# Performance work log

Hardware: AMD Instinct MI355X
Metric: run time of the kernel (lower is better)

The kernel has to match this reference:

```python
import jax, jax.numpy as jnp
import numpy as np

B = 2048   # structures
A = 512    # atoms per structure (constant)
N = B * A  # total atoms
O = 48     # symmetry operations


def setup_inputs() -> dict:
    key = jax.random.key(0)
    k1, k2, k3, k4, k5 = jax.random.split(key, 5)
    lattices = jax.random.normal(k1, (B, 3, 3), jnp.float32)
    inv_lattices = jax.random.normal(k2, (B, 3, 3), jnp.float32)
    forces = jax.random.normal(k3, (N, 3), jnp.float32)
    general_ops = jax.random.normal(k4, (O, 4, 4), jnp.float32)
    # scatter targets; in practice these permute atoms within a structure,
    # but any in-range index gives the same math/memory pattern
    symm_map = jax.random.randint(k5, (N, O), 0, N, dtype=jnp.int32)
    num_atoms = jnp.full((B,), A, dtype=jnp.int64)
    num_general_ops = jnp.full((B,), O, dtype=jnp.int64)
    return {
        "lattices": lattices,
        "inv_lattices": inv_lattices,
        "forces": forces,
        "num_atoms": num_atoms,
        "general_ops": general_ops,
        "symm_map": symm_map,
        "num_general_ops": num_general_ops,
    }


def reference(lattices, inv_lattices, forces, num_atoms, general_ops, symm_map, num_general_ops):
    n = forces.shape[0]
    # per-atom lattices via repeat_interleave(num_atoms)
    lat = jnp.repeat(lattices, num_atoms, axis=0, total_repeat_length=n)       # [N,3,3]
    inv_lat = jnp.repeat(inv_lattices, num_atoms, axis=0, total_repeat_length=n)
    # fractional (scaled) forces: einsum('nji,nj->ni')
    scaled = jnp.einsum('nji,nj->ni', inv_lat, forces)                          # [N,3]
    # apply every symmetry rotation at once (vectorized over the op loop)
    rot = general_ops[:, :3, :3]                                                # [O,3,3]
    transformed = jnp.einsum('oij,nj->oni', rot, scaled)                        # [O,N,3]
    # scatter-add each op's transformed forces to symm_map[:, iop] targets
    tgt = symm_map.T.reshape(-1)                                                # [O*N]
    acc = jnp.zeros_like(scaled).at[tgt].add(transformed.reshape(-1, 3))        # [N,3]
    # normalize by number of ops of each atom's structure
    counts = jnp.repeat(num_general_ops, num_atoms, axis=0, total_repeat_length=n)
    sym_scaled = acc / counts.astype(scaled.dtype)[:, None]
    # back to cartesian: einsum('nji,nj->ni') with lattices
    return jnp.einsum('nji,nj->ni', lat, sym_scaled)
```

## Files before the change

kernel.cpp:

```cpp
#include <hip/hip_runtime.h>
#include <math.h>

#define BLOCK 256
#define PBLOCK 1024
#define NB 256
#define TILE 4096
#define GP 512
#define KSLICE 4
#define KS_TOT (KSLICE + 1)
#define GPK (GP / KSLICE)
#define CAPS 27
#define ABLOCK 512
#define AWAVES (ABLOCK / 64)

__global__ void scan_offsets_kernel(const int* __restrict__ num_atoms, int B,
                                    int* __restrict__ offsets) {
    __shared__ long long partial[1024];
    int t = threadIdx.x;
    int per = (B + 1023) / 1024;
    int base_idx = t * per;
    long long local = 0;
    for (int i = 0; i < per; ++i) {
        int idx = base_idx + i;
        if (idx < B) local += num_atoms[idx];
    }
    partial[t] = local;
    __syncthreads();
    for (int d = 1; d < 1024; d <<= 1) {
        long long v = (t >= d) ? partial[t - d] : 0;
        __syncthreads();
        partial[t] += v;
        __syncthreads();
    }
    long long run = (t == 0) ? 0 : partial[t - 1];
    for (int i = 0; i < per; ++i) {
        int idx = base_idx + i;
        if (idx < B) {
            offsets[idx] = (int)run;
            run += num_atoms[idx];
        }
    }
    if (t == 1023) offsets[B] = (int)partial[1023];
}

__device__ __forceinline__ int find_batch(const int* __restrict__ offsets, int B, int n) {
    int lo = 0, hi = B;
    while (hi - lo > 1) {
        int mid = (lo + hi) >> 1;
        if (offsets[mid] <= n) lo = mid; else hi = mid;
    }
    return lo;
}

__global__ void scale_kernel(const float* __restrict__ inv_lat,
                             const float* __restrict__ forces,
                             const int* __restrict__ offsets, int B, int N,
                             float4* __restrict__ scaled, float* __restrict__ partials,
                             int zf, int zt) {
    int n = blockIdx.x * blockDim.x + threadIdx.x;
    if (n >= N) return;
    int b = find_batch(offsets, B, n);
    const float* M = inv_lat + (size_t)b * 9;
    float f0 = forces[n * 3 + 0], f1 = forces[n * 3 + 1], f2 = forces[n * 3 + 2];
    float s0 = M[0] * f0 + M[3] * f1 + M[6] * f2;
    float s1 = M[1] * f0 + M[4] * f1 + M[7] * f2;
    float s2 = M[2] * f0 + M[5] * f1 + M[8] * f2;
    scaled[n] = make_float4(s0, s1, s2, 0.f);
    for (int k = zf; k < zt; ++k) {
        float* a = partials + (size_t)k * N * 3;
        a[n * 3 + 0] = 0.f; a[n * 3 + 1] = 0.f; a[n * 3 + 2] = 0.f;
    }
}

__device__ __forceinline__ int bucket_of(int tgt, int N) {
    return (int)(((unsigned long long)(unsigned)tgt * (unsigned)NB) / (unsigned)N);
}

__global__ __launch_bounds__(PBLOCK, 8) void place_kernel(
                             const int* __restrict__ symm_map,
                             const float4* __restrict__ scaled,
                             const float* __restrict__ general_ops,
                             int atom_base, int atom_cnt, int N, int O, int cap,
                             uint2* __restrict__ records, int* __restrict__ cnts,
                             float* __restrict__ ovf) {
    __shared__ int scnt[NB];
    __shared__ int gcur[NB];
    __shared__ uint2 stage[NB * CAPS];
    int tid = threadIdx.x, g = blockIdx.x;
    int G = PBLOCK / O;
    int active = G * O;
    int grp = tid / O;
    int o = tid - grp * O;
    float r0 = 0, r1 = 0, r2 = 0, r3 = 0, r4 = 0, r5 = 0, r6 = 0, r7 = 0, r8 = 0;
    if (tid < active) {
        const float* Ro = general_ops + (size_t)o * 16;
        r0 = Ro[0]; r1 = Ro[1]; r2 = Ro[2];
        r3 = Ro[4]; r4 = Ro[5]; r5 = Ro[6];
        r6 = Ro[8]; r7 = Ro[9]; r8 = Ro[10];
    }
    for (int i = tid; i < NB; i += PBLOCK) {
        gcur[i] = (int)(((size_t)g * NB + i) * (size_t)cap);
        scnt[i] = 0;
    }
    __syncthreads();
    int apb = (atom_cnt + GP - 1) / GP;
    int a0 = atom_base + g * apb;
    int aend = atom_base + atom_cnt;
    int a1 = a0 + apb; if (a1 > aend) a1 = aend;
    int myAtoms = a1 - a0; if (myAtoms < 0) myAtoms = 0;
    int rstep = G * 4;
    int rounds = (myAtoms + rstep - 1) / rstep;

    for (int r = 0; r < rounds; ++r) {
        if (tid < active) {
            int abase = a0 + r * rstep + grp;
            #pragma unroll
            for (int j = 0; j < 4; ++j) {
                int a = abase + j * G;
                if (a < a1) {
                    int tgt = symm_map[(size_t)a * (size_t)O + (size_t)o];
                    float4 s = scaled[a];
                    float v0 = r0 * s.x + r1 * s.y + r2 * s.z;
                    float v1 = r3 * s.x + r4 * s.y + r5 * s.z;
                    float v2 = r6 * s.x + r7 * s.y + r8 * s.z;
                    float m = fmaxf(fmaxf(fabsf(v0), fabsf(v1)), fabsf(v2));
                    int bb = bucket_of(tgt, N);
                    bool done = false;
                    if (m < 15.9f) {
                        int pos = atomicAdd(&scnt[bb], 1);
                        if (pos < CAPS) {
                            unsigned q0 = (unsigned)(int)rintf(v0 * 32.f + 512.f);
                            unsigned q1 = (unsigned)(int)rintf(v1 * 32.f + 512.f);
                            unsigned q2 = (unsigned)(int)rintf(v2 * 32.f + 512.f);
                            stage[bb * CAPS + pos] =
                                make_uint2(q0 | (q1 << 16),
                                           q2 | (((unsigned)tgt & 0xFFFFu) << 16));
                            done = true;
                        }
                    }
                    if (!done) {
                        atomicAdd(&ovf[(size_t)tgt * 3 + 0], v0);
                        atomicAdd(&ovf[(size_t)tgt * 3 + 1], v1);
                        atomicAdd(&ovf[(size_t)tgt * 3 + 2], v2);
                    }
                }
            }
        }
        __syncthreads();
        int ib = tid >> 4;
        int j = tid & 15;
        for (int pass = 0; pass < NB; pass += PBLOCK / 16) {
            int ii = pass + ib;
            int c = scnt[ii]; if (c > CAPS) c = CAPS;
            int gb = gcur[ii];
            int lim = (int)(((size_t)g * NB + ii + 1) * (size_t)cap);
            int room = lim - gb;
            int w = (c < room) ? c : room; if (w < 0) w = 0;
            for (int k = j; k < w; k += 16)
                records[(size_t)gb + k] = stage[ii * CAPS + k];
            for (int k = w + j; k < c; k += 16) {
                uint2 f = stage[ii * CAPS + k];
                int lo = (int)(((long long)ii * N + NB - 1) / NB);
                int tgt = lo + ((((int)(f.y >> 16)) - (lo & 0xFFFF)) & 0xFFFF);
                float v0 = (float)((int)(f.x & 0xFFFF) - 512) * 0.03125f;
                float v1 = (float)((int)(f.x >> 16) - 512) * 0.03125f;
                float v2 = (float)((int)(f.y & 0xFFFF) - 512) * 0.03125f;
                atomicAdd(&ovf[(size_t)tgt * 3 + 0], v0);
                atomicAdd(&ovf[(size_t)tgt * 3 + 1], v1);
                atomicAdd(&ovf[(size_t)tgt * 3 + 2], v2);
            }
            if (j == 0) { gcur[ii] = gb + w; scnt[ii] = 0; }
        }
        __syncthreads();
    }
    for (int i = tid; i < NB; i += PBLOCK) {
        int base = (int)(((size_t)g * NB + i) * (size_t)cap);
        int c = gcur[i] - base;
        if (c > cap) c = cap;
        if (c < 0) c = 0;
        cnts[(size_t)g * NB + i] = c;
    }
}

__device__ __forceinline__ void accum_rec(unsigned long long* accL,
                                          unsigned x, unsigned y, int lo16) {
    int local = ((int)(y >> 16) - lo16) & 0xFFFF;
    unsigned long long u = (1ULL << 54)
                         | ((unsigned long long)(x & 0xFFFFu) << 36)
                         | ((unsigned long long)(x >> 16) << 18)
                         | (unsigned long long)(y & 0xFFFFu);
    (void)__hip_atomic_fetch_add(&accL[local], u, __ATOMIC_RELAXED, __HIP_MEMORY_SCOPE_WORKGROUP);
}

__global__ __launch_bounds__(ABLOCK) void accum_kernel(const uint2* __restrict__ records,
                             const int* __restrict__ cnts, int N, int cap,
                             float* __restrict__ partials, int store_mode) {
    __shared__ unsigned long long accL[TILE];
    int b = blockIdx.x / KSLICE;
    int k = blockIdx.x - b * KSLICE;
    int tid = threadIdx.x;
    int lo = (int)(((long long)b * N + NB - 1) / NB);
    int hi = (int)(((long long)(b + 1) * N + NB - 1) / NB);
    if (hi > N) hi = N;
    int span = hi - lo;
    for (int i = tid; i < span; i += ABLOCK) accL[i] = 0ULL;
    __syncthreads();
    int lo16 = lo & 0xFFFF;
    int g0 = k * GPK;
    int wave = tid >> 6;
    int lane = tid & 63;
    for (int g = g0 + wave; g < g0 + GPK; g += AWAVES) {
        int c = cnts[(size_t)g * NB + b];
        const uint2* r = records + ((size_t)g * NB + b) * (size_t)cap;
        const uint4* r4 = (const uint4*)r;
        int pairs = c >> 1;
        for (int i = lane; i < pairs; i += 64) {
            uint4 f = r4[i];
            accum_rec(accL, f.x, f.y, lo16);
            accum_rec(accL, f.z, f.w, lo16);
        }
        if (lane == 0 && (c & 1)) {
            uint2 f = r[c - 1];
            accum_rec(accL, f.x, f.y, lo16);
        }
    }
    __syncthreads();
    float* gp = partials + (size_t)k * N * 3 + (size_t)lo * 3;
    for (int t = tid; t < span; t += ABLOCK) {
        unsigned long long u = accL[t];
        int cc = (int)(unsigned)(u >> 54);
        int q0 = (int)((u >> 36) & 0x3FFFF);
        int q1 = (int)((u >> 18) & 0x3FFFF);
        int q2 = (int)(u & 0x3FFFF);
        float f0 = (float)(q0 - 512 * cc) * 0.03125f;
        float f1 = (float)(q1 - 512 * cc) * 0.03125f;
        float f2 = (float)(q2 - 512 * cc) * 0.03125f;
        if (store_mode) {
            gp[t * 3 + 0] = f0; gp[t * 3 + 1] = f1; gp[t * 3 + 2] = f2;
        } else {
            gp[t * 3 + 0] += f0; gp[t * 3 + 1] += f1; gp[t * 3 + 2] += f2;
        }
    }
}

__global__ void scatter_kernel(const float4* __restrict__ scaled,
                               const float* __restrict__ general_ops,
                               const int* __restrict__ symm_map,
                               float* __restrict__ acc,
                               long long total, int O) {
    long long t = (long long)blockIdx.x * blockDim.x + threadIdx.x;
    if (t >= total) return;
    long long n = t / O;
    int o = (int)(t - n * O);
    float4 s = scaled[n];
    const float* R = general_ops + (size_t)o * 16;
    float v0 = R[0] * s.x + R[1] * s.y + R[2] * s.z;
    float v1 = R[4] * s.x + R[5] * s.y + R[6] * s.z;
    float v2 = R[8] * s.x + R[9] * s.y + R[10] * s.z;
    int tgt = symm_map[t];
    atomicAdd(&acc[(size_t)tgt * 3 + 0], v0);
    atomicAdd(&acc[(size_t)tgt * 3 + 1], v1);
    atomicAdd(&acc[(size_t)tgt * 3 + 2], v2);
}

__global__ void output_kernel(const float* __restrict__ lat,
                              const int* __restrict__ num_general_ops,
                              const int* __restrict__ offsets, int B, int N,
                              const float* __restrict__ partials, int K,
                              float* __restrict__ out) {
    int n = blockIdx.x * blockDim.x + threadIdx.x;
    if (n >= N) return;
    int b = find_batch(offsets, B, n);
    float inv_cnt = 1.0f / (float)num_general_ops[b];
    float a0 = 0.f, a1 = 0.f, a2 = 0.f;
    for (int k = 0; k < K; ++k) {
        const float* a = partials + (size_t)k * N * 3;
        a0 += a[n * 3 + 0]; a1 += a[n * 3 + 1]; a2 += a[n * 3 + 2];
    }
    a0 *= inv_cnt; a1 *= inv_cnt; a2 *= inv_cnt;
    const float* M = lat + (size_t)b * 9;
    out[n * 3 + 0] = M[0] * a0 + M[3] * a1 + M[6] * a2;
    out[n * 3 + 1] = M[1] * a0 + M[4] * a1 + M[7] * a2;
    out[n * 3 + 2] = M[2] * a0 + M[5] * a1 + M[8] * a2;
}

static inline size_t align16(size_t x) { return (x + 15) & ~(size_t)15; }

extern "C" void kernel_launch(void* const* d_in, const int* in_sizes, int n_in,
                              void* d_out, int out_size, void* d_ws, size_t ws_size,
                              hipStream_t stream) {
    const float* lattices        = (const float*)d_in[0];
    const float* inv_lattices    = (const float*)d_in[1];
    const float* forces          = (const float*)d_in[2];
    const int*   num_atoms       = (const int*)d_in[3];
    const float* general_ops     = (const float*)d_in[4];
    const int*   symm_map        = (const int*)d_in[5];
    const int*   num_general_ops = (const int*)d_in[6];

    int B = in_sizes[0] / 9;
    int N = in_sizes[2] / 3;
    int O = in_sizes[4] / 16;
    long long total = (long long)N * O;

    char* p = (char*)d_ws;
    size_t used = 0;
    float4* scaled  = (float4*)(p + used); used = align16(used + (size_t)N * sizeof(float4));
    float* partials = (float*)(p + used);  used = align16(used + (size_t)KS_TOT * N * 3 * sizeof(float));
    int* offsets    = (int*)(p + used);    used = align16(used + (size_t)(B + 1) * sizeof(int));
    int* cnts       = (int*)(p + used);    used = align16(used + (size_t)NB * GP * sizeof(int));
    size_t remaining = (ws_size > used) ? ws_size - used : 0;

    int C = -1, cap = 0, chunk_atoms = 0;
    for (int c = 1; c <= 64; ++c) {
        int ca = (N + c - 1) / c;
        int apb = (ca + GP - 1) / GP;
        double m = (double)apb * (double)O / (double)NB;
        long long capc = (long long)(m + 5.0 * sqrt(m > 1.0 ? m : 1.0) + 16.0);
        capc = (capc + 7) & ~7LL;
        if ((size_t)NB * (size_t)GP * (size_t)capc * sizeof(uint2) <= remaining) {
            C = c; cap = (int)capc; chunk_atoms = ca; break;
        }
    }
    bool fast = (C > 0) && (((long long)N + NB - 1) / NB <= TILE) && (O <= 64)
                && (total < (1LL << 31))
                && ((long long)NB * GP * cap < (1LL << 31));

    int gridN = (N + BLOCK - 1) / BLOCK;
    scan_offsets_kernel<<<1, 1024, 0, stream>>>(num_atoms, B, offsets);

    if (fast) {
        uint2* records = (uint2*)(p + used);
        float* ovf = partials + (size_t)KSLICE * N * 3;
        int store_mode = (C == 1) ? 1 : 0;
        int zf = store_mode ? KSLICE : 0;
        scale_kernel<<<gridN, BLOCK, 0, stream>>>(inv_lattices, forces, offsets, B, N,
                                                  scaled, partials, zf, KS_TOT);
        for (int c = 0; c < C; ++c) {
            int abase = c * chunk_atoms;
            if (abase >= N) break;
            int acnt = N - abase;
            if (acnt > chunk_atoms) acnt = chunk_atoms;
            place_kernel<<<GP, PBLOCK, 0, stream>>>(symm_map, scaled, general_ops,
                                                    abase, acnt, N, O, cap,
                                                    records, cnts, ovf);
            accum_kernel<<<NB * KSLICE, ABLOCK, 0, stream>>>(records, cnts, N, cap,
                                                             partials, store_mode);
        }
        output_kernel<<<gridN, BLOCK, 0, stream>>>(lattices, num_general_ops, offsets, B, N,
                                                   partials, KS_TOT, (float*)d_out);
    } else {
        scale_kernel<<<gridN, BLOCK, 0, stream>>>(inv_lattices, forces, offsets, B, N,
                                                  scaled, partials, 0, 1);
        long long gridS = (total + BLOCK - 1) / BLOCK;
        scatter_kernel<<<(int)gridS, BLOCK, 0, stream>>>(scaled, general_ops, symm_map, partials, total, O);
        output_kernel<<<gridN, BLOCK, 0, stream>>>(lattices, num_general_ops, offsets, B, N,
                                                   partials, 1, (float*)d_out);
    }
}
```

Measured before the change: 670.1 us.

## Accumulate each chunk into its own slice and force at least five chunks

```diff
diff --git a/kernel.cpp b/kernel.cpp
--- a/kernel.cpp
+++ b/kernel.cpp
@@ -6,12 +6,9 @@
 #define NB 256
 #define TILE 4096
 #define GP 512
-#define KSLICE 4
-#define KS_TOT (KSLICE + 1)
-#define GPK (GP / KSLICE)
+#define KSMAX 8
 #define CAPS 27
-#define ABLOCK 512
-#define AWAVES (ABLOCK / 64)
+#define ABLOCK 1024
 
 __global__ void scan_offsets_kernel(const int* __restrict__ num_atoms, int B,
                                     int* __restrict__ offsets) {
@@ -194,10 +191,9 @@
 
 __global__ __launch_bounds__(ABLOCK) void accum_kernel(const uint2* __restrict__ records,
                              const int* __restrict__ cnts, int N, int cap,
-                             float* __restrict__ partials, int store_mode) {
+                             float* __restrict__ slice) {
     __shared__ unsigned long long accL[TILE];
-    int b = blockIdx.x / KSLICE;
-    int k = blockIdx.x - b * KSLICE;
+    int b = blockIdx.x;
     int tid = threadIdx.x;
     int lo = (int)(((long long)b * N + NB - 1) / NB);
     int hi = (int)(((long long)(b + 1) * N + NB - 1) / NB);
@@ -206,10 +202,10 @@
     for (int i = tid; i < span; i += ABLOCK) accL[i] = 0ULL;
     __syncthreads();
     int lo16 = lo & 0xFFFF;
-    int g0 = k * GPK;
     int wave = tid >> 6;
     int lane = tid & 63;
-    for (int g = g0 + wave; g < g0 + GPK; g += AWAVES) {
+    const int NW = ABLOCK / 64;
+    for (int g = wave; g < GP; g += NW) {
         int c = cnts[(size_t)g * NB + b];
         const uint2* r = records + ((size_t)g * NB + b) * (size_t)cap;
         const uint4* r4 = (const uint4*)r;
@@ -225,21 +221,16 @@
         }
     }
     __syncthreads();
-    float* gp = partials + (size_t)k * N * 3 + (size_t)lo * 3;
+    float* gp = slice + (size_t)lo * 3;
     for (int t = tid; t < span; t += ABLOCK) {
         unsigned long long u = accL[t];
         int cc = (int)(unsigned)(u >> 54);
         int q0 = (int)((u >> 36) & 0x3FFFF);
         int q1 = (int)((u >> 18) & 0x3FFFF);
         int q2 = (int)(u & 0x3FFFF);
-        float f0 = (float)(q0 - 512 * cc) * 0.03125f;
-        float f1 = (float)(q1 - 512 * cc) * 0.03125f;
-        float f2 = (float)(q2 - 512 * cc) * 0.03125f;
-        if (store_mode) {
-            gp[t * 3 + 0] = f0; gp[t * 3 + 1] = f1; gp[t * 3 + 2] = f2;
-        } else {
-            gp[t * 3 + 0] += f0; gp[t * 3 + 1] += f1; gp[t * 3 + 2] += f2;
-        }
+        gp[t * 3 + 0] = (float)(q0 - 512 * cc) * 0.03125f;
+        gp[t * 3 + 1] = (float)(q1 - 512 * cc) * 0.03125f;
+        gp[t * 3 + 2] = (float)(q2 - 512 * cc) * 0.03125f;
     }
 }
 
@@ -305,13 +296,13 @@
     char* p = (char*)d_ws;
     size_t used = 0;
     float4* scaled  = (float4*)(p + used); used = align16(used + (size_t)N * sizeof(float4));
-    float* partials = (float*)(p + used);  used = align16(used + (size_t)KS_TOT * N * 3 * sizeof(float));
+    float* partials = (float*)(p + used);  used = align16(used + (size_t)(KSMAX + 1) * N * 3 * sizeof(float));
     int* offsets    = (int*)(p + used);    used = align16(used + (size_t)(B + 1) * sizeof(int));
     int* cnts       = (int*)(p + used);    used = align16(used + (size_t)NB * GP * sizeof(int));
     size_t remaining = (ws_size > used) ? ws_size - used : 0;
 
     int C = -1, cap = 0, chunk_atoms = 0;
-    for (int c = 1; c <= 64; ++c) {
+    for (int c = 5; c <= KSMAX; ++c) {
         int ca = (N + c - 1) / c;
         int apb = (ca + GP - 1) / GP;
         double m = (double)apb * (double)O / (double)NB;
@@ -330,11 +321,9 @@
 
     if (fast) {
         uint2* records = (uint2*)(p + used);
-        float* ovf = partials + (size_t)KSLICE * N * 3;
-        int store_mode = (C == 1) ? 1 : 0;
-        int zf = store_mode ? KSLICE : 0;
+        float* ovf = partials + (size_t)C * N * 3;
         scale_kernel<<<gridN, BLOCK, 0, stream>>>(inv_lattices, forces, offsets, B, N,
-                                                  scaled, partials, zf, KS_TOT);
+                                                  scaled, partials, C, C + 1);
         for (int c = 0; c < C; ++c) {
             int abase = c * chunk_atoms;
             if (abase >= N) break;
@@ -343,11 +332,11 @@
             place_kernel<<<GP, PBLOCK, 0, stream>>>(symm_map, scaled, general_ops,
                                                     abase, acnt, N, O, cap,
                                                     records, cnts, ovf);
-            accum_kernel<<<NB * KSLICE, ABLOCK, 0, stream>>>(records, cnts, N, cap,
-                                                             partials, store_mode);
+            accum_kernel<<<NB, ABLOCK, 0, stream>>>(records, cnts, N, cap,
+                                                    partials + (size_t)c * N * 3);
         }
         output_kernel<<<gridN, BLOCK, 0, stream>>>(lattices, num_general_ops, offsets, B, N,
-                                                   partials, KS_TOT, (float*)d_out);
+                                                   partials, C + 1, (float*)d_out);
     } else {
         scale_kernel<<<gridN, BLOCK, 0, stream>>>(inv_lattices, forces, offsets, B, N,
                                                   scaled, partials, 0, 1);
```

After: 773.3 us. +15.4%, slower.
